# Optimization experiments

Measured on AMD Instinct MI355X. Metric: run time of the kernel, lower is better.

Reference implementation:

```python
import jax, jax.numpy as jnp
import numpy as np

IN_CH = 128
HID = 256   # 2 * out_channels
OUT_CH = 128
N_NODES = 10000
N_EDGES = 640000


def setup_inputs() -> dict:
    key = jax.random.key(0)
    ks = jax.random.split(key, 6)
    x = jax.random.normal(ks[0], (N_NODES, IN_CH), dtype=jnp.float32)
    edge_index = jax.random.randint(ks[1], (2, N_EDGES), 0, N_NODES, dtype=jnp.int64)
    # GCNConv params (glorot-like scale)
    W1 = jax.random.normal(ks[2], (IN_CH, HID), dtype=jnp.float32) / np.sqrt(IN_CH)
    b1 = jnp.zeros((HID,), dtype=jnp.float32)
    W2 = jax.random.normal(ks[3], (HID, OUT_CH), dtype=jnp.float32) / np.sqrt(HID)
    b2 = jnp.zeros((OUT_CH,), dtype=jnp.float32)
    return {"x": x, "edge_index": edge_index, "W1": W1, "b1": b1, "W2": W2, "b2": b2}


def _gcn_norm(edge_index, n_nodes):
    """Add self-loops and compute symmetric GCN normalization per edge."""
    loops = jnp.arange(n_nodes, dtype=edge_index.dtype)
    src = jnp.concatenate([edge_index[0], loops])  # [E+N]
    dst = jnp.concatenate([edge_index[1], loops])
    deg = jax.ops.segment_sum(jnp.ones_like(dst, dtype=jnp.float32), dst,
                              num_segments=n_nodes)
    dinv = jnp.where(deg > 0, jax.lax.rsqrt(deg), 0.0)
    norm = dinv[src] * dinv[dst]  # [E+N]
    return src, dst, norm


def _gcn_layer(x, W, b, src, dst, norm, n_nodes):
    h = x @ W                                  # [N, F_out]
    msg = h[src] * norm[:, None]               # gather + scale, [E+N, F_out]
    agg = jax.ops.segment_sum(msg, dst, num_segments=n_nodes)
    return agg + b


def reference(x, edge_index, W1, b1, W2, b2):
    n = x.shape[0]
    src, dst, norm = _gcn_norm(edge_index, n)
    h = jax.nn.relu(_gcn_layer(x, W1, b1, src, dst, norm, n))
    out = jax.nn.relu(_gcn_layer(h, W2, b2, src, dst, norm, n))
    return out
```

## Files before the change

kernel.cpp:

```cpp
#include <hip/hip_runtime.h>

#define N_FEAT 128
#define HID 256
#define OUT_CH 128

#define NB 256
#define NJ 40
#define MAXN 10240

typedef unsigned short u16;
typedef _Float16 f16x8 __attribute__((ext_vector_type(8)));
typedef float f32x4 __attribute__((ext_vector_type(4)));

__device__ __forceinline__ unsigned pack_f16x2(float lo, float hi) {
    union { _Float16 h[2]; unsigned u; } c;
    c.h[0] = (_Float16)lo;
    c.h[1] = (_Float16)hi;
    return c.u;
}
__device__ __forceinline__ float2 unpack_f16x2(unsigned u) {
    union { unsigned u; _Float16 h[2]; } c;
    c.u = u;
    return make_float2((float)c.h[0], (float)c.h[1]);
}
__device__ __forceinline__ u16 f16u(float f) {
    union { _Float16 h; u16 u; } c;
    c.h = (_Float16)f;
    return c.u;
}


__global__ __launch_bounds__(256)
void hist_kernel(const int* __restrict__ dst, u16* __restrict__ bh,
                 int* __restrict__ flag, int E, int N, int chunk) {
    __shared__ int hist[MAXN];
    if (blockIdx.x == 0 && threadIdx.x < 64) flag[threadIdx.x] = 0;
    for (int i = threadIdx.x; i < N; i += 256) hist[i] = 0;
    __syncthreads();
    int base = blockIdx.x * chunk;
    int lim = min(chunk, E - base);
    for (int i = threadIdx.x; i < lim; i += 256) {
        int d = dst[base + i];
        if (d >= 0 && d < N) atomicAdd(&hist[d], 1);
    }
    __syncthreads();
    u16* out = bh + (size_t)blockIdx.x * N;
    for (int i = threadIdx.x; i < N; i += 256) out[i] = (u16)hist[i];
}

__global__ __launch_bounds__(256)
void colscan_scan_kernel(u16* __restrict__ bh, int* __restrict__ row_start,
                         float* __restrict__ dinv, int* __restrict__ flag,
                         int N) {
    int tid = threadIdx.x;
    int b = blockIdx.x;
    int j = b * 256 + tid;
    int run = 0;
    if (j < N) {
        #pragma unroll 8
        for (int bb = 0; bb < NB; bb++) {
            size_t idx = (size_t)bb * N + j;
            int t = bh[idx];
            bh[idx] = (u16)run;
            run += t;
        }
        dinv[j] = rsqrtf((float)(run + 1));
    }
    __shared__ int wsum[4];
    __shared__ int sbase;
    int lane = tid & 63, wv = tid >> 6;
    int incl = run;
    #pragma unroll
    for (int off = 1; off < 64; off <<= 1) {
        int t = __shfl_up(incl, off, 64);
        if (lane >= off) incl += t;
    }
    if (lane == 63) wsum[wv] = incl;
    __syncthreads();
    int wbase = 0;
    #pragma unroll
    for (int k = 0; k < 4; k++)
        if (k < wv) wbase += wsum[k];
    int local_excl = wbase + (incl - run);
    int T_b = wsum[0] + wsum[1] + wsum[2] + wsum[3];
    if (tid == 0)
        __hip_atomic_store(&flag[b], T_b + 1, __ATOMIC_RELAXED,
                           __HIP_MEMORY_SCOPE_AGENT);
    if (tid < 64) {
        int v = 0;
        if (tid < b) {
            int f;
            do {
                f = __hip_atomic_load(&flag[tid], __ATOMIC_RELAXED,
                                      __HIP_MEMORY_SCOPE_AGENT);
            } while (f == 0);
            v = f - 1;
        }
        #pragma unroll
        for (int off = 1; off < 64; off <<= 1) v += __shfl_xor(v, off, 64);
        if (tid == 0) sbase = v;
    }
    __syncthreads();
    int base = sbase;
    if (j < N) row_start[j] = base + local_excl;
    if (b == NJ - 1 && tid == 0) row_start[N] = base + T_b;
}

__global__ __launch_bounds__(256)
void scat_kernel(const int* __restrict__ src, const int* __restrict__ dst,
                 const u16* __restrict__ bh,
                 const int* __restrict__ row_start,
                 int* __restrict__ csr_src,
                 const float* __restrict__ x, const float* __restrict__ dinv,
                 unsigned* __restrict__ xs_b,
                 const float* __restrict__ W1, const float* __restrict__ W2,
                 u16* __restrict__ W1t, u16* __restrict__ W2t,
                 int E, int N, int chunk) {
    __shared__ int cur[MAXN];
    const u16* basep = bh + (size_t)blockIdx.x * N;
    for (int i = threadIdx.x; i < N; i += 256)
        cur[i] = row_start[i] + (int)basep[i];
    __syncthreads();
    int base = blockIdx.x * chunk;
    int lim = min(chunk, E - base);
    for (int i = threadIdx.x; i < lim; i += 256) {
        int e = base + i;
        int d = dst[e];
        if (d < 0 || d >= N) continue;
        int pos = atomicAdd(&cur[d], 1);
        if ((unsigned)pos < (unsigned)E) csr_src[pos] = src[e];
    }
    const int total4 = N * N_FEAT / 4;
    const int stride = NB * 256;
    int g0 = blockIdx.x * 256 + threadIdx.x;
    for (int i = g0; i < total4; i += stride) {
        int row = i >> 5;
        float d = dinv[row];
        float4 v = ((const float4*)x)[i];
        uint2 p;
        p.x = pack_f16x2(v.x * d, v.y * d);
        p.y = pack_f16x2(v.z * d, v.w * d);
        ((uint2*)xs_b)[i] = p;
    }
    const int TOTW = N_FEAT * HID + HID * OUT_CH;
    for (int t = g0; t < TOTW; t += stride) {
        if (t < N_FEAT * HID) {
            int n = t >> 7, k = t & 127;
            W1t[t] = f16u(W1[(size_t)k * HID + n]);
        } else {
            int j2 = t - N_FEAT * HID;
            int n = j2 >> 8, k = j2 & 255;
            W2t[j2] = f16u(W2[(size_t)k * OUT_CH + n]);
        }
    }
}

__device__ __forceinline__ void agg_tail(const unsigned* __restrict__ featb,
                                         const int* __restrict__ csr_src,
                                         int e, int e1, int f,
                                         float& accx, float& accy) {
    for (; e + 4 <= e1; e += 4) {
        int s0 = csr_src[e], s1 = csr_src[e + 1];
        int s2 = csr_src[e + 2], s3 = csr_src[e + 3];
        unsigned w0 = featb[(size_t)s0 * 64 + f];
        unsigned w1 = featb[(size_t)s1 * 64 + f];
        unsigned w2 = featb[(size_t)s2 * 64 + f];
        unsigned w3 = featb[(size_t)s3 * 64 + f];
        float2 u0 = unpack_f16x2(w0), u1 = unpack_f16x2(w1);
        float2 u2 = unpack_f16x2(w2), u3 = unpack_f16x2(w3);
        accx += u0.x + u1.x + u2.x + u3.x;
        accy += u0.y + u1.y + u2.y + u3.y;
    }
    for (; e < e1; ++e) {
        float2 u = unpack_f16x2(featb[(size_t)csr_src[e] * 64 + f]);
        accx += u.x;
        accy += u.y;
    }
}

__device__ __forceinline__ void agg_full(const unsigned* __restrict__ featb,
                                         const int* __restrict__ csr_src,
                                         int e, int e1, int f,
                                         float& accx, float& accy) {
    if (e + 8 <= e1) {
        int s_cur[8];
        #pragma unroll
        for (int j = 0; j < 8; j++) s_cur[j] = csr_src[e + j];
        e += 8;
        for (; e + 8 <= e1; e += 8) {
            unsigned w[8];
            #pragma unroll
            for (int j = 0; j < 8; j++) w[j] = featb[(size_t)s_cur[j] * 64 + f];
            int s_nxt[8];
            #pragma unroll
            for (int j = 0; j < 8; j++) s_nxt[j] = csr_src[e + j];
            #pragma unroll
            for (int j = 0; j < 8; j++) {
                float2 u = unpack_f16x2(w[j]);
                accx += u.x;
                accy += u.y;
            }
            #pragma unroll
            for (int j = 0; j < 8; j++) s_cur[j] = s_nxt[j];
        }
        unsigned w[8];
        #pragma unroll
        for (int j = 0; j < 8; j++) w[j] = featb[(size_t)s_cur[j] * 64 + f];
        #pragma unroll
        for (int j = 0; j < 8; j++) {
            float2 u = unpack_f16x2(w[j]);
            accx += u.x;
            accy += u.y;
        }
    }
    agg_tail(featb, csr_src, e, e1, f, accx, accy);
}

template <bool EPILOGUE, bool F16OUT>
__global__ __launch_bounds__(256)
void agg_kernel(const unsigned* __restrict__ featb,
                const float* __restrict__ dinv,
                const int* __restrict__ row_start,
                const int* __restrict__ csr_src,
                const float* __restrict__ bias,
                void* __restrict__ out, int N) {
    int wave = threadIdx.x >> 6;
    int f = threadIdx.x & 63;
    int na = blockIdx.x * 8 + wave * 2;
    if (na >= N) return;
    int nb = na + 1;
    bool hasB = (nb < N);

    float2 va = unpack_f16x2(featb[(size_t)na * 64 + f]);
    float ax = va.x, ay = va.y;
    float bx = 0.f, by = 0.f;
    if (hasB) {
        float2 vb = unpack_f16x2(featb[(size_t)nb * 64 + f]);
        bx = vb.x;
        by = vb.y;
    }
    int ea = row_start[na], ea1 = row_start[na + 1];
    int eb = 0, eb1 = 0;
    if (hasB) { eb = ea1; eb1 = row_start[nb + 1]; }

    if (hasB && ea + 8 <= ea1 && eb + 8 <= eb1) {
        int sa[8], sb[8];
        #pragma unroll
        for (int j = 0; j < 8; j++) sa[j] = csr_src[ea + j];
        #pragma unroll
        for (int j = 0; j < 8; j++) sb[j] = csr_src[eb + j];
        ea += 8;
        eb += 8;
        while (ea + 8 <= ea1 && eb + 8 <= eb1) {
            unsigned wa[8], wb[8];
            #pragma unroll
            for (int j = 0; j < 8; j++) wa[j] = featb[(size_t)sa[j] * 64 + f];
            #pragma unroll
            for (int j = 0; j < 8; j++) wb[j] = featb[(size_t)sb[j] * 64 + f];
            int sna[8], snb[8];
            #pragma unroll
            for (int j = 0; j < 8; j++) sna[j] = csr_src[ea + j];
            #pragma unroll
            for (int j = 0; j < 8; j++) snb[j] = csr_src[eb + j];
            #pragma unroll
            for (int j = 0; j < 8; j++) {
                float2 u = unpack_f16x2(wa[j]);
                ax += u.x;
                ay += u.y;
            }
            #pragma unroll
            for (int j = 0; j < 8; j++) {
                float2 u = unpack_f16x2(wb[j]);
                bx += u.x;
                by += u.y;
            }
            #pragma unroll
            for (int j = 0; j < 8; j++) {
                sa[j] = sna[j];
                sb[j] = snb[j];
            }
            ea += 8;
            eb += 8;
        }
        unsigned wa[8], wb[8];
        #pragma unroll
        for (int j = 0; j < 8; j++) wa[j] = featb[(size_t)sa[j] * 64 + f];
        #pragma unroll
        for (int j = 0; j < 8; j++) wb[j] = featb[(size_t)sb[j] * 64 + f];
        #pragma unroll
        for (int j = 0; j < 8; j++) {
            float2 u = unpack_f16x2(wa[j]);
            ax += u.x;
            ay += u.y;
        }
        #pragma unroll
        for (int j = 0; j < 8; j++) {
            float2 u = unpack_f16x2(wb[j]);
            bx += u.x;
            by += u.y;
        }
        agg_full(featb, csr_src, ea, ea1, f, ax, ay);
        agg_full(featb, csr_src, eb, eb1, f, bx, by);
    } else {
        agg_full(featb, csr_src, ea, ea1, f, ax, ay);
        if (hasB) agg_full(featb, csr_src, eb, eb1, f, bx, by);
    }

    float dna = dinv[na];
    ax *= dna;
    ay *= dna;
    float2 bias2 = make_float2(0.f, 0.f);
    if (EPILOGUE) {
        bias2 = ((const float2*)bias)[f];
        ax = fmaxf(ax + bias2.x, 0.0f);
        ay = fmaxf(ay + bias2.y, 0.0f);
    }
    if (F16OUT) {
        ((unsigned*)out)[(size_t)na * 64 + f] = pack_f16x2(ax, ay);
    } else {
        float2 r;
        r.x = ax;
        r.y = ay;
        ((float2*)out)[(size_t)na * 64 + f] = r;
    }
    if (hasB) {
        float dnb = dinv[nb];
        bx *= dnb;
        by *= dnb;
        if (EPILOGUE) {
            bx = fmaxf(bx + bias2.x, 0.0f);
            by = fmaxf(by + bias2.y, 0.0f);
        }
        if (F16OUT) {
            ((unsigned*)out)[(size_t)nb * 64 + f] = pack_f16x2(bx, by);
        } else {
            float2 r;
            r.x = bx;
            r.y = by;
            ((float2*)out)[(size_t)nb * 64 + f] = r;
        }
    }
}

__global__ __launch_bounds__(256)
void mlp_kernel(const u16* __restrict__ A,
                const u16* __restrict__ W1t,
                const u16* __restrict__ W2t,
                const float* __restrict__ b1,
                const float* __restrict__ rscale,
                u16* __restrict__ C,
                int M) {
    __shared__ __align__(16) u16 As[64 * 128];
    __shared__ __align__(16) u16 Wl[256 * 128];
    __shared__ __align__(16) u16 Hl[64 * 256];
    int tid = threadIdx.x;
    int w = tid >> 6;
    int l = tid & 63;
    int m0 = blockIdx.x * 64;
    int g = l >> 4;
    int cl = l & 15;

    for (int q = tid; q < 1024; q += 256) {
        int r = q >> 4, c = q & 15;
        *(f16x8*)&As[r * 128 + ((c ^ (r & 15)) * 8)] =
            *(const f16x8*)(A + (size_t)(m0 + r) * 128 + c * 8);
    }
    for (int q = tid; q < 4096; q += 256) {
        int r = q >> 4, c = q & 15;
        *(f16x8*)&Wl[r * 128 + ((c ^ (r & 15)) * 8)] =
            *(const f16x8*)(W1t + (size_t)r * 128 + c * 8);
    }
    __syncthreads();

    {
        f32x4 acc[16];
        const f32x4 zero = {0.f, 0.f, 0.f, 0.f};
        #pragma unroll
        for (int nf = 0; nf < 16; nf++) acc[nf] = zero;
        int rowA = w * 16 + cl;
        #pragma unroll
        for (int kc = 0; kc < 4; kc++) {
            int ch = kc * 4 + g;
            f16x8 af = *(const f16x8*)&As[rowA * 128 + ((ch ^ (rowA & 15)) * 8)];
            #pragma unroll
            for (int nf = 0; nf < 16; nf++) {
                int rb = nf * 16 + cl;
                f16x8 bf = *(const f16x8*)&Wl[rb * 128 + ((ch ^ (rb & 15)) * 8)];
                acc[nf] = __builtin_amdgcn_mfma_f32_16x16x32_f16(af, bf, acc[nf], 0, 0, 0);
            }
        }
        int r0 = g * 4;
        #pragma unroll
        for (int nf = 0; nf < 16; nf++) {
            int col = nf * 16 + cl;
            float bb = b1[col];
            #pragma unroll
            for (int r = 0; r < 4; r++) {
                int lr = w * 16 + r0 + r;
                float v = fmaxf(acc[nf][r] + bb, 0.0f);
                int cc = col >> 3;
                Hl[lr * 256 + ((cc ^ (lr & 31)) * 8) + (col & 7)] = f16u(v);
            }
        }
    }
    __syncthreads();

    for (int q = tid; q < 4096; q += 256) {
        int r = q >> 5, c = q & 31;
        *(f16x8*)&Wl[r * 256 + ((c ^ (r & 31)) * 8)] =
            *(const f16x8*)(W2t + (size_t)r * 256 + c * 8);
    }
    __syncthreads();

    {
        f32x4 acc[8];
        const f32x4 zero = {0.f, 0.f, 0.f, 0.f};
        #pragma unroll
        for (int nf = 0; nf < 8; nf++) acc[nf] = zero;
        int rowA = w * 16 + cl;
        #pragma unroll
        for (int kc = 0; kc < 8; kc++) {
            int ch = kc * 4 + g;
            f16x8 af = *(const f16x8*)&Hl[rowA * 256 + ((ch ^ (rowA & 31)) * 8)];
            #pragma unroll
            for (int nf = 0; nf < 8; nf++) {
                int rb = nf * 16 + cl;
                f16x8 bf = *(const f16x8*)&Wl[rb * 256 + ((ch ^ (rb & 31)) * 8)];
                acc[nf] = __builtin_amdgcn_mfma_f32_16x16x32_f16(af, bf, acc[nf], 0, 0, 0);
            }
        }
        int r0 = g * 4;
        #pragma unroll
        for (int r = 0; r < 4; r++) {
            int m = m0 + w * 16 + r0 + r;
            if (m >= M) continue;
            float rs = rscale[m];
            #pragma unroll
            for (int nf = 0; nf < 8; nf++) {
                int col = nf * 16 + cl;
                C[(size_t)m * 128 + col] = f16u(acc[nf][r] * rs);
            }
        }
    }
}


static inline size_t align512(size_t x) { return (x + 511) & ~(size_t)511; }

extern "C" void kernel_launch(void* const* d_in, const int* in_sizes, int n_in,
                              void* d_out, int out_size, void* d_ws, size_t ws_size,
                              hipStream_t stream) {
    const float* x = (const float*)d_in[0];
    const int* ei = (const int*)d_in[1];
    const float* W1 = (const float*)d_in[2];
    const float* b1 = (const float*)d_in[3];
    const float* W2 = (const float*)d_in[4];
    const float* b2 = (const float*)d_in[5];
    float* out = (float*)d_out;

    const int N = in_sizes[0] / N_FEAT;
    const int E = in_sizes[1] / 2;
    const int* src = ei;
    const int* dst = ei + E;

    const int Mpad = ((N + 63) / 64) * 64;

    char* ws = (char*)d_ws;
    size_t off = 0;
    float* dinv = (float*)(ws + off);    off += align512((size_t)N * 4);
    int* flag = (int*)(ws + off);        off += align512((size_t)64 * 4);
    int* row_start = (int*)(ws + off);   off += align512((size_t)(N + 1) * 4);
    int* csr_src = (int*)(ws + off);     off += align512((size_t)E * 4);
    unsigned* xs_b = (unsigned*)(ws + off);  off += align512((size_t)N * 64 * 4);
    u16* agg1h = (u16*)(ws + off);       off += align512((size_t)Mpad * N_FEAT * 2);
    u16* t16 = (u16*)(ws + off);         off += align512((size_t)N * OUT_CH * 2);
    u16* W1t = (u16*)(ws + off);         off += align512((size_t)HID * N_FEAT * 2);
    u16* W2t = (u16*)(ws + off);         off += align512((size_t)OUT_CH * HID * 2);
    u16* bh = (u16*)(ws + off);          off += align512((size_t)NB * N * 2);
    (void)ws_size;
    const int chunk = (E + NB - 1) / NB;

    hist_kernel<<<NB, 256, 0, stream>>>(dst, bh, flag, E, N, chunk);
    colscan_scan_kernel<<<NJ, 256, 0, stream>>>(bh, row_start, dinv, flag, N);
    scat_kernel<<<NB, 256, 0, stream>>>(src, dst, bh, row_start, csr_src,
                                        x, dinv, xs_b, W1, W2, W1t, W2t,
                                        E, N, chunk);

    agg_kernel<false, true><<<(N + 7) / 8, 256, 0, stream>>>(
        xs_b, dinv, row_start, csr_src, nullptr, agg1h, N);

    mlp_kernel<<<Mpad / 64, 256, 0, stream>>>(agg1h, W1t, W2t, b1, dinv, t16, N);

    agg_kernel<true, false><<<(N + 7) / 8, 256, 0, stream>>>(
        (const unsigned*)t16, dinv, row_start, csr_src, b2, out, N);
}
```

Measured before the change: 174.6 us.

## Replace per-block histogram CSR build with global atomic counting and cursors

Replaces the per-block LDS histogram plus column-scan CSR construction with a single global atomic count of destination degrees, a scan over those counts, and a scatter that uses global atomic cursors. This drops the 256xN u16 histogram buffer and its serial column scan, at the cost of contended global atomics and nondeterministic edge order within each CSR row. It also switches gather indexing from 64-bit multiplies to 32-bit shifts, which may reduce address arithmetic.

```diff
diff --git a/kernel.cpp b/kernel.cpp
--- a/kernel.cpp
+++ b/kernel.cpp
@@ -4,9 +4,8 @@
 #define HID 256
 #define OUT_CH 128
 
-#define NB 256
 #define NJ 40
-#define MAXN 10240
+#define CSR_B 1280
 
 typedef unsigned short u16;
 typedef _Float16 f16x8 __attribute__((ext_vector_type(8)));
@@ -31,39 +30,25 @@
 
 
 __global__ __launch_bounds__(256)
-void hist_kernel(const int* __restrict__ dst, u16* __restrict__ bh,
-                 int* __restrict__ flag, int E, int N, int chunk) {
-    __shared__ int hist[MAXN];
-    if (blockIdx.x == 0 && threadIdx.x < 64) flag[threadIdx.x] = 0;
-    for (int i = threadIdx.x; i < N; i += 256) hist[i] = 0;
-    __syncthreads();
-    int base = blockIdx.x * chunk;
-    int lim = min(chunk, E - base);
-    for (int i = threadIdx.x; i < lim; i += 256) {
-        int d = dst[base + i];
-        if (d >= 0 && d < N) atomicAdd(&hist[d], 1);
-    }
-    __syncthreads();
-    u16* out = bh + (size_t)blockIdx.x * N;
-    for (int i = threadIdx.x; i < N; i += 256) out[i] = (u16)hist[i];
+void count_kernel(const int* __restrict__ dst, int* __restrict__ counts,
+                  int E, int N) {
+    int stride = gridDim.x * 256;
+    for (int i = blockIdx.x * 256 + threadIdx.x; i < E; i += stride) {
+        int d = dst[i];
+        if ((unsigned)d < (unsigned)N) atomicAdd(&counts[d], 1);
+    }
 }
 
 __global__ __launch_bounds__(256)
-void colscan_scan_kernel(u16* __restrict__ bh, int* __restrict__ row_start,
-                         float* __restrict__ dinv, int* __restrict__ flag,
-                         int N) {
+void scan40_kernel(const int* __restrict__ counts, int* __restrict__ row_start,
+                   int* __restrict__ cursor, float* __restrict__ dinv,
+                   int* __restrict__ flag, int N) {
     int tid = threadIdx.x;
     int b = blockIdx.x;
     int j = b * 256 + tid;
     int run = 0;
     if (j < N) {
-        #pragma unroll 8
-        for (int bb = 0; bb < NB; bb++) {
-            size_t idx = (size_t)bb * N + j;
-            int t = bh[idx];
-            bh[idx] = (u16)run;
-            run += t;
-        }
+        run = counts[j];
         dinv[j] = rsqrtf((float)(run + 1));
     }
     __shared__ int wsum[4];
@@ -102,37 +87,32 @@
     }
     __syncthreads();
     int base = sbase;
-    if (j < N) row_start[j] = base + local_excl;
+    if (j < N) {
+        int rs = base + local_excl;
+        row_start[j] = rs;
+        cursor[j] = rs;
+    }
     if (b == NJ - 1 && tid == 0) row_start[N] = base + T_b;
 }
 
 __global__ __launch_bounds__(256)
 void scat_kernel(const int* __restrict__ src, const int* __restrict__ dst,
-                 const u16* __restrict__ bh,
-                 const int* __restrict__ row_start,
-                 int* __restrict__ csr_src,
+                 int* __restrict__ cursor, int* __restrict__ csr_src,
                  const float* __restrict__ x, const float* __restrict__ dinv,
                  unsigned* __restrict__ xs_b,
                  const float* __restrict__ W1, const float* __restrict__ W2,
                  u16* __restrict__ W1t, u16* __restrict__ W2t,
-                 int E, int N, int chunk) {
-    __shared__ int cur[MAXN];
-    const u16* basep = bh + (size_t)blockIdx.x * N;
-    for (int i = threadIdx.x; i < N; i += 256)
-        cur[i] = row_start[i] + (int)basep[i];
-    __syncthreads();
-    int base = blockIdx.x * chunk;
-    int lim = min(chunk, E - base);
-    for (int i = threadIdx.x; i < lim; i += 256) {
-        int e = base + i;
+                 int E, int N) {
+    const int stride = gridDim.x * 256;
+    int g0 = blockIdx.x * 256 + threadIdx.x;
+    for (int e = g0; e < E; e += stride) {
         int d = dst[e];
-        if (d < 0 || d >= N) continue;
-        int pos = atomicAdd(&cur[d], 1);
-        if ((unsigned)pos < (unsigned)E) csr_src[pos] = src[e];
+        if ((unsigned)d < (unsigned)N) {
+            int pos = atomicAdd(&cursor[d], 1);
+            if ((unsigned)pos < (unsigned)E) csr_src[pos] = src[e];
+        }
     }
     const int total4 = N * N_FEAT / 4;
-    const int stride = NB * 256;
-    int g0 = blockIdx.x * 256 + threadIdx.x;
     for (int i = g0; i < total4; i += stride) {
         int row = i >> 5;
         float d = dinv[row];
@@ -162,17 +142,17 @@
     for (; e + 4 <= e1; e += 4) {
         int s0 = csr_src[e], s1 = csr_src[e + 1];
         int s2 = csr_src[e + 2], s3 = csr_src[e + 3];
-        unsigned w0 = featb[(size_t)s0 * 64 + f];
-        unsigned w1 = featb[(size_t)s1 * 64 + f];
-        unsigned w2 = featb[(size_t)s2 * 64 + f];
-        unsigned w3 = featb[(size_t)s3 * 64 + f];
+        unsigned w0 = featb[((unsigned)s0 << 6) + f];
+        unsigned w1 = featb[((unsigned)s1 << 6) + f];
+        unsigned w2 = featb[((unsigned)s2 << 6) + f];
+        unsigned w3 = featb[((unsigned)s3 << 6) + f];
         float2 u0 = unpack_f16x2(w0), u1 = unpack_f16x2(w1);
         float2 u2 = unpack_f16x2(w2), u3 = unpack_f16x2(w3);
         accx += u0.x + u1.x + u2.x + u3.x;
         accy += u0.y + u1.y + u2.y + u3.y;
     }
     for (; e < e1; ++e) {
-        float2 u = unpack_f16x2(featb[(size_t)csr_src[e] * 64 + f]);
+        float2 u = unpack_f16x2(featb[((unsigned)csr_src[e] << 6) + f]);
         accx += u.x;
         accy += u.y;
     }
@@ -190,7 +170,7 @@
         for (; e + 8 <= e1; e += 8) {
             unsigned w[8];
             #pragma unroll
-            for (int j = 0; j < 8; j++) w[j] = featb[(size_t)s_cur[j] * 64 + f];
+            for (int j = 0; j < 8; j++) w[j] = featb[((unsigned)s_cur[j] << 6) + f];
             int s_nxt[8];
             #pragma unroll
             for (int j = 0; j < 8; j++) s_nxt[j] = csr_src[e + j];
@@ -205,7 +185,7 @@
         }
         unsigned w[8];
         #pragma unroll
-        for (int j = 0; j < 8; j++) w[j] = featb[(size_t)s_cur[j] * 64 + f];
+        for (int j = 0; j < 8; j++) w[j] = featb[((unsigned)s_cur[j] << 6) + f];
         #pragma unroll
         for (int j = 0; j < 8; j++) {
             float2 u = unpack_f16x2(w[j]);
@@ -231,11 +211,11 @@
     int nb = na + 1;
     bool hasB = (nb < N);
 
-    float2 va = unpack_f16x2(featb[(size_t)na * 64 + f]);
+    float2 va = unpack_f16x2(featb[((unsigned)na << 6) + f]);
     float ax = va.x, ay = va.y;
     float bx = 0.f, by = 0.f;
     if (hasB) {
-        float2 vb = unpack_f16x2(featb[(size_t)nb * 64 + f]);
+        float2 vb = unpack_f16x2(featb[((unsigned)nb << 6) + f]);
         bx = vb.x;
         by = vb.y;
     }
@@ -254,9 +234,9 @@
         while (ea + 8 <= ea1 && eb + 8 <= eb1) {
             unsigned wa[8], wb[8];
             #pragma unroll
-            for (int j = 0; j < 8; j++) wa[j] = featb[(size_t)sa[j] * 64 + f];
-            #pragma unroll
-            for (int j = 0; j < 8; j++) wb[j] = featb[(size_t)sb[j] * 64 + f];
+            for (int j = 0; j < 8; j++) wa[j] = featb[((unsigned)sa[j] << 6) + f];
+            #pragma unroll
+            for (int j = 0; j < 8; j++) wb[j] = featb[((unsigned)sb[j] << 6) + f];
             int sna[8], snb[8];
             #pragma unroll
             for (int j = 0; j < 8; j++) sna[j] = csr_src[ea + j];
@@ -284,9 +264,9 @@
         }
         unsigned wa[8], wb[8];
         #pragma unroll
-        for (int j = 0; j < 8; j++) wa[j] = featb[(size_t)sa[j] * 64 + f];
-        #pragma unroll
-        for (int j = 0; j < 8; j++) wb[j] = featb[(size_t)sb[j] * 64 + f];
+        for (int j = 0; j < 8; j++) wa[j] = featb[((unsigned)sa[j] << 6) + f];
+        #pragma unroll
+        for (int j = 0; j < 8; j++) wb[j] = featb[((unsigned)sb[j] << 6) + f];
         #pragma unroll
         for (int j = 0; j < 8; j++) {
             float2 u = unpack_f16x2(wa[j]);
@@ -316,12 +296,12 @@
         ay = fmaxf(ay + bias2.y, 0.0f);
     }
     if (F16OUT) {
-        ((unsigned*)out)[(size_t)na * 64 + f] = pack_f16x2(ax, ay);
+        ((unsigned*)out)[((unsigned)na << 6) + f] = pack_f16x2(ax, ay);
     } else {
         float2 r;
         r.x = ax;
         r.y = ay;
-        ((float2*)out)[(size_t)na * 64 + f] = r;
+        ((float2*)out)[((unsigned)na << 6) + f] = r;
     }
     if (hasB) {
         float dnb = dinv[nb];
@@ -332,12 +312,12 @@
             by = fmaxf(by + bias2.y, 0.0f);
         }
         if (F16OUT) {
-            ((unsigned*)out)[(size_t)nb * 64 + f] = pack_f16x2(bx, by);
+            ((unsigned*)out)[((unsigned)nb << 6) + f] = pack_f16x2(bx, by);
         } else {
             float2 r;
             r.x = bx;
             r.y = by;
-            ((float2*)out)[(size_t)nb * 64 + f] = r;
+            ((float2*)out)[((unsigned)nb << 6) + f] = r;
         }
     }
 }
@@ -468,23 +448,23 @@
     char* ws = (char*)d_ws;
     size_t off = 0;
     float* dinv = (float*)(ws + off);    off += align512((size_t)N * 4);
-    int* flag = (int*)(ws + off);        off += align512((size_t)64 * 4);
+    int* counts = (int*)(ws + off);      off += align512((size_t)(N + 64) * 4);
+    int* flag = counts + N;
     int* row_start = (int*)(ws + off);   off += align512((size_t)(N + 1) * 4);
+    int* cursor = (int*)(ws + off);      off += align512((size_t)N * 4);
     int* csr_src = (int*)(ws + off);     off += align512((size_t)E * 4);
     unsigned* xs_b = (unsigned*)(ws + off);  off += align512((size_t)N * 64 * 4);
     u16* agg1h = (u16*)(ws + off);       off += align512((size_t)Mpad * N_FEAT * 2);
     u16* t16 = (u16*)(ws + off);         off += align512((size_t)N * OUT_CH * 2);
     u16* W1t = (u16*)(ws + off);         off += align512((size_t)HID * N_FEAT * 2);
     u16* W2t = (u16*)(ws + off);         off += align512((size_t)OUT_CH * HID * 2);
-    u16* bh = (u16*)(ws + off);          off += align512((size_t)NB * N * 2);
     (void)ws_size;
-    const int chunk = (E + NB - 1) / NB;
-
-    hist_kernel<<<NB, 256, 0, stream>>>(dst, bh, flag, E, N, chunk);
-    colscan_scan_kernel<<<NJ, 256, 0, stream>>>(bh, row_start, dinv, flag, N);
-    scat_kernel<<<NB, 256, 0, stream>>>(src, dst, bh, row_start, csr_src,
-                                        x, dinv, xs_b, W1, W2, W1t, W2t,
-                                        E, N, chunk);
+
+    hipMemsetAsync(counts, 0, (size_t)(N + 64) * 4, stream);
+    count_kernel<<<CSR_B, 256, 0, stream>>>(dst, counts, E, N);
+    scan40_kernel<<<NJ, 256, 0, stream>>>(counts, row_start, cursor, dinv, flag, N);
+    scat_kernel<<<CSR_B, 256, 0, stream>>>(src, dst, cursor, csr_src,
+                                           x, dinv, xs_b, W1, W2, W1t, W2t, E, N);
 
     agg_kernel<false, true><<<(N + 7) / 8, 256, 0, stream>>>(
         xs_b, dinv, row_start, csr_src, nullptr, agg1h, N);
```

Measured after the change: 200.9 us. 15.1% more time.
